# Kernel tuning notes

Measured on AMD Instinct MI355X. Metric: run time of the kernel, lower is better.

The kernel has to match this reference:

```python
import jax, jax.numpy as jnp
import numpy as np

_EPS = 1e-10
_SHIFT = 1


def setup_inputs() -> dict:
    key = jax.random.key(0)
    k1, k2 = jax.random.split(key)
    n_rays, n_samples = 262144, 128
    alpha = jax.random.uniform(k1, (n_rays, n_samples), dtype=jnp.float32)
    rgbs = jax.random.uniform(k2, (n_rays, n_samples, 3), dtype=jnp.float32)
    return {"alpha": alpha, "rgbs": rgbs}


def reference(alpha, rgbs):
    # transmittance: cumulative product of (1 - alpha + eps) along samples
    trans = jnp.cumprod(1.0 - alpha + _EPS, axis=-1)
    # shift right by _SHIFT and fill the first _SHIFT entries with 1
    # (equivalent to torch.roll + trans[..., :shift] = 1 for shift <= n_samples)
    ones = jnp.ones(alpha.shape[:-1] + (_SHIFT,), dtype=alpha.dtype)
    trans = jnp.concatenate([ones, trans[..., :-_SHIFT]], axis=-1)
    weights = trans * alpha  # [n_rays, n_samples]
    # weighted sum over samples -> rendered rgb [n_rays, 3]
    rgbs_rendered = jnp.einsum("rs,rsc->rc", weights, rgbs)
    return rgbs_rendered
```

## Files before the change

kernel.cpp:

```cpp
#include <hip/hip_runtime.h>

#define N_SAMPLES 128
#define EPS 1e-10f

typedef float f4 __attribute__((ext_vector_type(4)));

__global__ __launch_bounds__(256) void VolumeRenderer_14336600834233_kernel(
    const f4* __restrict__ alpha4,
    const f4* __restrict__ rgb4,
    float* __restrict__ out,
    int n_rays)
{
    const int wavesPerBlock = blockDim.x >> 6;
    const int wave = blockIdx.x * wavesPerBlock + (threadIdx.x >> 6);
    const int lane = threadIdx.x & 63;
    const int g    = lane >> 5;
    const int l    = lane & 31;
    const int ray  = wave * 2 + g;
    if (ray >= n_rays) return;

    const f4 av = alpha4[(size_t)ray * 32 + l];
    const float f0 = 1.0f - av.x + EPS;
    const float f1 = 1.0f - av.y + EPS;
    const float f2 = 1.0f - av.z + EPS;
    const float f3 = 1.0f - av.w + EPS;
    const float p  = (f0 * f1) * (f2 * f3);

    float incl = p;
    #pragma unroll
    for (int off = 1; off < 32; off <<= 1) {
        float v = __shfl_up(incl, off, 64);
        incl = (l >= off) ? incl * v : incl;
    }
    float excl = __shfl_up(incl, 1, 64);
    if (l == 0) excl = 1.0f;

    const float w0 = av.x * excl;
    const float t1 = excl * f0;
    const float w1 = av.y * t1;
    const float t2 = t1 * f1;
    const float w2 = av.z * t2;
    const float w3 = av.w * (t2 * f2);

    const size_t rb = (size_t)ray * 96 + (size_t)l * 3;
    const f4 x0 = rgb4[rb + 0];
    const f4 x1 = rgb4[rb + 1];
    const f4 x2 = rgb4[rb + 2];

    float cr = fmaf(w0, x0.x, fmaf(w1, x0.w, fmaf(w2, x1.z, w3 * x2.y)));
    float cg = fmaf(w0, x0.y, fmaf(w1, x1.x, fmaf(w2, x1.w, w3 * x2.z)));
    float cb = fmaf(w0, x0.z, fmaf(w1, x1.y, fmaf(w2, x2.x, w3 * x2.w)));

    #pragma unroll
    for (int off = 16; off; off >>= 1) {
        cr += __shfl_xor(cr, off, 64);
        cg += __shfl_xor(cg, off, 64);
        cb += __shfl_xor(cb, off, 64);
    }

    if (l == 0) {
        float* o = out + (size_t)ray * 3;
        o[0] = cr;
        o[1] = cg;
        o[2] = cb;
    }
}

extern "C" void kernel_launch(void* const* d_in, const int* in_sizes, int n_in,
                              void* d_out, int out_size, void* d_ws, size_t ws_size,
                              hipStream_t stream) {
    const f4* alpha4 = (const f4*)d_in[0];
    const f4* rgb4   = (const f4*)d_in[1];
    float* out = (float*)d_out;

    const int n_rays = in_sizes[0] / N_SAMPLES;

    const int block = 256;
    const int rays_per_block = (block / 64) * 2;
    const int grid = (n_rays + rays_per_block - 1) / rays_per_block;

    VolumeRenderer_14336600834233_kernel<<<grid, block, 0, stream>>>(
        alpha4, rgb4, out, n_rays);
}
```

Measured before the change: 95.08 us.

## Use persistent grid-stride waves with software-prefetched next ray pair

Replaces the one-wave-per-ray-pair launch with a fixed grid of 2048 blocks whose waves loop over ray pairs with a grid stride. Each iteration issues the loads for the next pair before computing the current one, so memory latency overlaps with the scan and reduction. This trades fewer in-flight waves and higher register pressure for explicit prefetching. It also drops handling of an odd ray count, since n_pairs uses floor division.

Result: slower. 104.0 us (+9.3%).

```diff
diff --git a/kernel.cpp b/kernel.cpp
--- a/kernel.cpp
+++ b/kernel.cpp
@@ -9,60 +9,81 @@
     const f4* __restrict__ alpha4,
     const f4* __restrict__ rgb4,
     float* __restrict__ out,
-    int n_rays)
+    int n_pairs)
 {
     const int wavesPerBlock = blockDim.x >> 6;
-    const int wave = blockIdx.x * wavesPerBlock + (threadIdx.x >> 6);
+    const int nWaves = gridDim.x * wavesPerBlock;
     const int lane = threadIdx.x & 63;
     const int g    = lane >> 5;
     const int l    = lane & 31;
-    const int ray  = wave * 2 + g;
-    if (ray >= n_rays) return;
 
-    const f4 av = alpha4[(size_t)ray * 32 + l];
-    const float f0 = 1.0f - av.x + EPS;
-    const float f1 = 1.0f - av.y + EPS;
-    const float f2 = 1.0f - av.z + EPS;
-    const float f3 = 1.0f - av.w + EPS;
-    const float p  = (f0 * f1) * (f2 * f3);
+    int pair = blockIdx.x * wavesPerBlock + (threadIdx.x >> 6);
+    if (pair >= n_pairs) return;
 
-    float incl = p;
-    #pragma unroll
-    for (int off = 1; off < 32; off <<= 1) {
-        float v = __shfl_up(incl, off, 64);
-        incl = (l >= off) ? incl * v : incl;
-    }
-    float excl = __shfl_up(incl, 1, 64);
-    if (l == 0) excl = 1.0f;
+    int ray = pair * 2 + g;
+    f4 av = alpha4[(size_t)ray * 32 + l];
+    size_t rb = (size_t)ray * 96 + (size_t)l * 3;
+    f4 x0 = rgb4[rb + 0];
+    f4 x1 = rgb4[rb + 1];
+    f4 x2 = rgb4[rb + 2];
 
-    const float w0 = av.x * excl;
-    const float t1 = excl * f0;
-    const float w1 = av.y * t1;
-    const float t2 = t1 * f1;
-    const float w2 = av.z * t2;
-    const float w3 = av.w * (t2 * f2);
+    while (true) {
+        const int npair = pair + nWaves;
+        const bool more = npair < n_pairs;
+        f4 nav, nx0, nx1, nx2;
+        if (more) {
+            const int nray = npair * 2 + g;
+            nav = alpha4[(size_t)nray * 32 + l];
+            const size_t nrb = (size_t)nray * 96 + (size_t)l * 3;
+            nx0 = rgb4[nrb + 0];
+            nx1 = rgb4[nrb + 1];
+            nx2 = rgb4[nrb + 2];
+        }
 
-    const size_t rb = (size_t)ray * 96 + (size_t)l * 3;
-    const f4 x0 = rgb4[rb + 0];
-    const f4 x1 = rgb4[rb + 1];
-    const f4 x2 = rgb4[rb + 2];
+        const float f0 = 1.0f - av.x + EPS;
+        const float f1 = 1.0f - av.y + EPS;
+        const float f2 = 1.0f - av.z + EPS;
+        const float f3 = 1.0f - av.w + EPS;
+        const float p  = (f0 * f1) * (f2 * f3);
 
-    float cr = fmaf(w0, x0.x, fmaf(w1, x0.w, fmaf(w2, x1.z, w3 * x2.y)));
-    float cg = fmaf(w0, x0.y, fmaf(w1, x1.x, fmaf(w2, x1.w, w3 * x2.z)));
-    float cb = fmaf(w0, x0.z, fmaf(w1, x1.y, fmaf(w2, x2.x, w3 * x2.w)));
+        float incl = p;
+        #pragma unroll
+        for (int off = 1; off < 32; off <<= 1) {
+            float v = __shfl_up(incl, off, 64);
+            incl = (l >= off) ? incl * v : incl;
+        }
+        float excl = __shfl_up(incl, 1, 64);
+        if (l == 0) excl = 1.0f;
 
-    #pragma unroll
-    for (int off = 16; off; off >>= 1) {
-        cr += __shfl_xor(cr, off, 64);
-        cg += __shfl_xor(cg, off, 64);
-        cb += __shfl_xor(cb, off, 64);
-    }
+        const float w0 = av.x * excl;
+        const float t1 = excl * f0;
+        const float w1 = av.y * t1;
+        const float t2 = t1 * f1;
+        const float w2 = av.z * t2;
+        const float w3 = av.w * (t2 * f2);
 
-    if (l == 0) {
-        float* o = out + (size_t)ray * 3;
-        o[0] = cr;
-        o[1] = cg;
-        o[2] = cb;
+        float cr = fmaf(w0, x0.x, fmaf(w1, x0.w, fmaf(w2, x1.z, w3 * x2.y)));
+        float cg = fmaf(w0, x0.y, fmaf(w1, x1.x, fmaf(w2, x1.w, w3 * x2.z)));
+        float cb = fmaf(w0, x0.z, fmaf(w1, x1.y, fmaf(w2, x2.x, w3 * x2.w)));
+
+        #pragma unroll
+        for (int off = 16; off; off >>= 1) {
+            cr += __shfl_xor(cr, off, 64);
+            cg += __shfl_xor(cg, off, 64);
+            cb += __shfl_xor(cb, off, 64);
+        }
+
+        if (l == 0) {
+            const int oray = pair * 2 + g;
+            float* o = out + (size_t)oray * 3;
+            o[0] = cr;
+            o[1] = cg;
+            o[2] = cb;
+        }
+
+        if (!more) break;
+        pair = npair;
+        av = nav; x0 = nx0; x1 = nx1; x2 = nx2;
     }
 }
 
@@ -73,12 +94,12 @@
     const f4* rgb4   = (const f4*)d_in[1];
     float* out = (float*)d_out;
 
-    const int n_rays = in_sizes[0] / N_SAMPLES;
+    const int n_rays  = in_sizes[0] / N_SAMPLES;
+    const int n_pairs = n_rays / 2;
 
     const int block = 256;
-    const int rays_per_block = (block / 64) * 2;
-    const int grid = (n_rays + rays_per_block - 1) / rays_per_block;
+    const int grid  = 2048;
 
     VolumeRenderer_14336600834233_kernel<<<grid, block, 0, stream>>>(
-        alpha4, rgb4, out, n_rays);
+        alpha4, rgb4, out, n_pairs);
 }
```
